# Optimization experiments

Hardware: AMD Instinct MI355X
Metric: run time of the kernel (lower is better)

The kernel has to match this reference:

```python
import jax, jax.numpy as jnp
import numpy as np
from jax import lax

KERNEL = 512

def squash(x, axis=-1):
    sn = jnp.sum(x * x, axis=axis, keepdims=True)
    scale = sn / (1.0 + sn)
    return scale * x / jnp.sqrt(sn + 1e-8)

def setup_inputs() -> dict:
    key = jax.random.key(0)
    ks = jax.random.split(key, 6)
    x = jax.random.normal(ks[0], (4096, 1, 1008), dtype=jnp.float32)
    a = jax.random.uniform(ks[1], (128, 1, 1), dtype=jnp.float32) * 5.0 + 0.1
    w = jax.random.uniform(ks[2], (128, 1, 1), dtype=jnp.float32) * 150.0 + 1.0
    conv_w = jax.random.normal(ks[3], (256, 128, 16), dtype=jnp.float32) * 0.02
    conv_b = jnp.zeros((256,), dtype=jnp.float32)
    W_caps = jax.random.normal(ks[4], (288, 4, 16, 8), dtype=jnp.float32) * 0.01
    return {"x": x, "a": a, "w": w, "conv_w": conv_w, "conv_b": conv_b, "W_caps": W_caps}

def reference(x, a, w, conv_w, conv_b, W_caps):
    # --- WavConv1d: generate wavelet weights on the fly ---
    t = jnp.linspace(-1.0, 1.0, KERNEL, dtype=jnp.float32).reshape(1, 1, KERNEL)
    a_safe = jnp.clip(a, 1e-5, None)
    t_scaled = t / a_safe
    wav_w = jnp.cos(w * t) * jnp.exp(-0.5 * t_scaled ** 2)  # [128,1,512]
    h = lax.conv_general_dilated(x, wav_w, window_strides=(16,), padding='VALID',
                                 dimension_numbers=('NCH', 'OIH', 'NCH'))  # [B,128,32]
    # --- PrimaryCaps1d ---
    p = lax.conv_general_dilated(h, conv_w, window_strides=(2,), padding='VALID',
                                 dimension_numbers=('NCH', 'OIH', 'NCH'))  # [B,256,9]
    p = p + conv_b[None, :, None]
    B = p.shape[0]
    u = squash(p.reshape(B, -1, 8))  # [B,288,8]
    # --- ClassCaps with dynamic routing ---
    # u_hat[b,c,d,o] = sum_i W_caps[c,d,o,i] * u[b,c,i]
    u_hat = jnp.einsum('cdoi,bci->bcdo', W_caps, u)  # [B,288,4,16]
    b_ij = jnp.zeros((B, u_hat.shape[1], u_hat.shape[2], 1), dtype=u_hat.dtype)
    num_routing = 3
    for i in range(num_routing):
        c_ij = jax.nn.softmax(b_ij, axis=2)                      # [B,288,4,1]
        s_j = jnp.sum(c_ij * u_hat, axis=1, keepdims=True)       # [B,1,4,16]
        v_j = squash(s_j, axis=-1)                               # [B,1,4,16]
        if i < num_routing - 1:
            agreement = jnp.sum(u_hat * v_j, axis=-1, keepdims=True)
            b_ij = b_ij + agreement
    v = jnp.squeeze(v_j, axis=1)          # [B,4,16]
    probs = jnp.linalg.norm(v, axis=-1)   # [B,4]
    return probs, jnp.squeeze(c_ij, axis=-1)  # [B,4], [B,288,4]
```

## Files before the change

### kernel.cpp

```cpp
#include <hip/hip_runtime.h>
#include <hip/hip_bf16.h>
#include <math.h>

typedef __attribute__((ext_vector_type(4))) short short4v;
typedef __attribute__((ext_vector_type(8))) short short8;
typedef __attribute__((ext_vector_type(4))) float f32x4;
typedef __attribute__((ext_vector_type(2))) float f32x2;
typedef _Float16 half8 __attribute__((ext_vector_type(8)));

#define BATCH   4096
#define XLEN    1008
#define NOC1    128
#define NPOS    32
#define NOC2    256
#define NQ      9
#define NCAPS   288
#define NDIM    8

#define BWH_OFF   0
#define BPH_OFF   131072
#define H2_OFF    1179648
#define U_OFF     34734080

static __device__ __forceinline__ short f2h(float v) {
    _Float16 h = (_Float16)v;
    return *reinterpret_cast<short*>(&h);
}

static __device__ __forceinline__ f32x2 pkfma(float a, f32x2 b, f32x2 c) {
    f32x2 av = {a, a};
    return av * b + c;
}

template <int CTRL>
static __device__ __forceinline__ float dpp_addf(float x) {
    int y = __builtin_amdgcn_update_dpp(0, __builtin_bit_cast(int, x),
                                        CTRL, 0xf, 0xf, true);
    return x + __builtin_bit_cast(float, y);
}
static __device__ __forceinline__ float rowsum16(float x) {
    x = dpp_addf<0xB1>(x);
    x = dpp_addf<0x4E>(x);
    x = dpp_addf<0x141>(x);
    x = dpp_addf<0x140>(x);
    return x;
}

__global__ __launch_bounds__(256) void k_pack(const float* __restrict__ a,
                                              const float* __restrict__ w,
                                              const float* __restrict__ cw,
                                              short* __restrict__ bwh,
                                              short* __restrict__ bph) {
    int bid = blockIdx.x;
    int tid = threadIdx.x;
    if (bid < 256) {
        int idx = bid * 256 + tid;
        int e    = idx & 7;
        int lane = (idx >> 3) & 63;
        int s    = (idx >> 9) & 15;
        int nt   = idx >> 13;
        int oc = nt * 16 + (lane & 15);
        int k  = s * 32 + (lane >> 4) * 8 + e;
        float t  = -1.0f + 2.0f * (float)k / 511.0f;
        float av = fmaxf(a[oc], 1e-5f);
        float ts = t / av;
        bwh[idx] = f2h(cosf(w[oc] * t) * expf(-0.5f * ts * ts));
    } else {
        int o = (bid - 256) * 256 + tid;
        int e    = o & 7;
        int lane = (o >> 3) & 63;
        int s    = (o >> 9) & 63;
        int nt   = o >> 15;
        int n  = nt * 16 + (lane & 15);
        int j  = lane >> 4;
        int kk = s >> 2;
        int ic = (s & 3) * 32 + j * 8 + e;
        bph[o] = f2h(cw[(n * NOC1 + ic) * 16 + kk]);
    }
}

__global__ __launch_bounds__(256, 2) void k_wavconv_mfma(
        const float* __restrict__ x,
        const short* __restrict__ bwh,
        short* __restrict__ h2) {
    __shared__ short xl[8][1512];

    int tid = threadIdx.x;
    int b0  = blockIdx.x * 8;

    for (int i4 = tid; i4 < 2016; i4 += 256) {
        int b  = i4 / 252;
        int e4 = i4 - b * 252;
        float4 v = *(const float4*)(x + (size_t)(b0 + b) * XLEN + e4 * 4);
        int i    = e4 * 4;
        int slot = i + 8 * (i >> 4);
        short4v hv;
        hv.x = f2h(v.x); hv.y = f2h(v.y); hv.z = f2h(v.z); hv.w = f2h(v.w);
        *(short4v*)&xl[b][slot] = hv;
    }
    __syncthreads();

    int lane = tid & 63;
    int w    = tid >> 6;
    int col  = lane & 15;
    int rg   = lane >> 4;

    f32x4 acc[4][8];
    f32x4 z = {0.f, 0.f, 0.f, 0.f};
#pragma unroll
    for (int tl = 0; tl < 4; ++tl)
#pragma unroll
        for (int nt = 0; nt < 8; ++nt) acc[tl][nt] = z;

    for (int s = 0; s < 16; ++s) {
        half8 Bh[8];
#pragma unroll
        for (int nt = 0; nt < 8; ++nt) {
            size_t off = ((size_t)(nt * 16 + s) * 64 + lane) * 8;
            Bh[nt] = __builtin_bit_cast(half8, *(const short8*)(bwh + off));
        }
#pragma unroll
        for (int tl = 0; tl < 4; ++tl) {
            int mt  = 4 * w + tl;
            int bl  = mt >> 1;
            int pos = (mt & 1) * 16 + col;
            int i    = (pos + 2 * s) * 16 + rg * 8;
            int slot = i + 8 * (i >> 4);
            half8 ah = __builtin_bit_cast(half8, *(const short8*)&xl[bl][slot]);
#pragma unroll
            for (int nt = 0; nt < 8; ++nt)
                acc[tl][nt] = __builtin_amdgcn_mfma_f32_16x16x32_f16(ah, Bh[nt], acc[tl][nt], 0, 0, 0);
        }
    }

#pragma unroll
    for (int tl = 0; tl < 4; ++tl) {
        int mt = 4 * w + tl;
        int b  = b0 + (mt >> 1);
        int ph = (mt & 1) * 16;
#pragma unroll
        for (int nt = 0; nt < 8; ++nt) {
            int oc = nt * 16 + col;
#pragma unroll
            for (int r = 0; r < 4; ++r) {
                int pos = ph + rg * 4 + r;
                h2[((size_t)b * NPOS + pos) * NOC1 + oc] = f2h(acc[tl][nt][r]);
            }
        }
    }
}

__global__ __launch_bounds__(512, 4) void k_conv_mfma(const short* __restrict__ h2,
                                                      const short* __restrict__ bph,
                                                      const float* __restrict__ cb,
                                                      float* __restrict__ u) {
    __shared__ char smem[66048];
    short* Ald   = (short*)smem;
    float* p_lds = (float*)smem;

    int tid  = threadIdx.x;
    int w    = tid >> 6;
    int lane = tid & 63;
    int col  = lane & 15;
    int rg   = lane >> 4;
    int b0   = blockIdx.x * 8;

    {
        const short8* src = (const short8*)(h2 + (size_t)b0 * NPOS * NOC1);
#pragma unroll
        for (int i = 0; i < 8; ++i) {
            int g    = tid + 512 * i;
            short8 v = src[g];
            int row  = g >> 4;
            int slot = (g & 15) ^ ((row >> 5) & 7);
            *(short8*)&Ald[row * 128 + slot * 8] = v;
        }
        if (tid < 32) {
            short8 zz = {0, 0, 0, 0, 0, 0, 0, 0};
            *(short8*)&Ald[4096 * 8 + tid * 8] = zz;
        }
    }
    __syncthreads();

    f32x4 acc[5][2];
    f32x4 z = {0.f, 0.f, 0.f, 0.f};
#pragma unroll
    for (int mt = 0; mt < 5; ++mt) { acc[mt][0] = z; acc[mt][1] = z; }

    int rowb[5];
#pragma unroll
    for (int mt = 0; mt < 5; ++mt) {
        int m = mt * 16 + col;
        rowb[mt] = (m & 7) * 32 + 2 * (m >> 3);
    }

    for (int s = 0; s < 64; ++s) {
        int kk    = s >> 2;
        int icb8  = (s & 3) * 4;
        short8 ar[5];
#pragma unroll
        for (int mt = 0; mt < 5; ++mt) {
            int row  = rowb[mt] + kk;
            int slot = (icb8 + rg) ^ ((row >> 5) & 7);
            ar[mt] = *(const short8*)&Ald[row * 128 + slot * 8];
        }
#pragma unroll
        for (int n = 0; n < 2; ++n) {
            size_t bo = ((size_t)((w + n * 8) * 64 + s) * 64 + lane) * 8;
            half8 Bh = __builtin_bit_cast(half8, *(const short8*)(bph + bo));
#pragma unroll
            for (int mt = 0; mt < 5; ++mt)
                acc[mt][n] = __builtin_amdgcn_mfma_f32_16x16x32_f16(
                    __builtin_bit_cast(half8, ar[mt]), Bh, acc[mt][n], 0, 0, 0);
        }
    }
    __syncthreads();

    int oc2l = w * 16 + col;
    for (int n = 0; n < 2; ++n) {
        float bias = cb[n * 128 + oc2l];
#pragma unroll
        for (int mt = 0; mt < 5; ++mt)
#pragma unroll
            for (int r = 0; r < 4; ++r) {
                int m = mt * 16 + rg * 4 + r;
                if (m < 72)
                    p_lds[(m & 7) * 1152 + oc2l * 9 + (m >> 3)] = acc[mt][n][r] + bias;
            }
        __syncthreads();
        for (int idx = tid; idx < 1152; idx += 512) {
            int lb = idx / 144;
            int cl = idx - lb * 144;
            float* ppt = &p_lds[lb * 1152 + cl * 8];
            float sn = 0.f;
#pragma unroll
            for (int i = 0; i < NDIM; ++i) sn = fmaf(ppt[i], ppt[i], sn);
            float sc = sn / (1.f + sn) / sqrtf(sn + 1e-8f);
            float* ug = u + ((size_t)(b0 + lb) * (NCAPS * NDIM) + (n * 144 + cl) * 8);
            float4 u0 = make_float4(ppt[0] * sc, ppt[1] * sc, ppt[2] * sc, ppt[3] * sc);
            float4 u1 = make_float4(ppt[4] * sc, ppt[5] * sc, ppt[6] * sc, ppt[7] * sc);
            ((float4*)ug)[0] = u0;
            ((float4*)ug)[1] = u1;
        }
        __syncthreads();
    }
}

__global__ __launch_bounds__(1024, 8) void k_routing(const float* __restrict__ u,
                                                     const float* __restrict__ Wc,
                                                     float* __restrict__ out) {
    __shared__ float b_lds[2][NCAPS * 4];
    __shared__ float c_lds[2][NCAPS * 4];
    __shared__ float s_lds[3][2][64];

    int tid = threadIdx.x;
    int b0  = blockIdx.x * 2;

    int g = tid >> 6;
    int l = tid & 63;
    int d = l >> 4;
    int o = l & 15;
    int gu = __builtin_amdgcn_readfirstlane(g);

    if (tid < 384) ((float*)s_lds)[tid] = 0.f;

    const float* ub0 = u + (size_t)(b0 + 0) * (NCAPS * NDIM) + gu * 18 * NDIM;
    const float* ub1 = u + (size_t)(b0 + 1) * (NCAPS * NDIM) + gu * 18 * NDIM;

    f32x2 uh[18];
#pragma unroll
    for (int c = 0; c < 18; ++c) {
        int cap = gu * 18 + c;
        const float4* W4 = (const float4*)(Wc + ((size_t)cap * 512) + l * 8);
        float4 A  = W4[0];
        float4 Bv = W4[1];
        f32x2 u0 = {ub0[c * 8 + 0], ub1[c * 8 + 0]};
        f32x2 u1 = {ub0[c * 8 + 1], ub1[c * 8 + 1]};
        f32x2 u2 = {ub0[c * 8 + 2], ub1[c * 8 + 2]};
        f32x2 u3 = {ub0[c * 8 + 3], ub1[c * 8 + 3]};
        f32x2 u4 = {ub0[c * 8 + 4], ub1[c * 8 + 4]};
        f32x2 u5 = {ub0[c * 8 + 5], ub1[c * 8 + 5]};
        f32x2 u6 = {ub0[c * 8 + 6], ub1[c * 8 + 6]};
        f32x2 u7 = {ub0[c * 8 + 7], ub1[c * 8 + 7]};
        f32x2 t = (f32x2){A.x, A.x} * u0;
        t = pkfma(A.y,  u1, t);
        t = pkfma(A.z,  u2, t);
        t = pkfma(A.w,  u3, t);
        t = pkfma(Bv.x, u4, t);
        t = pkfma(Bv.y, u5, t);
        t = pkfma(Bv.z, u6, t);
        t = pkfma(Bv.w, u7, t);
        uh[c] = t;
    }

    __syncthreads();

    for (int r = 0; r < 3; ++r) {
        if (r > 0) {
            __builtin_amdgcn_wave_barrier();
            for (int i = l; i < 36; i += 64) {
                int bb = (i >= 18) ? 1 : 0;
                int cl = i - bb * 18;
                int c  = gu * 18 + cl;
                float4 bv = *(const float4*)&b_lds[bb][c * 4];
                float m  = fmaxf(fmaxf(bv.x, bv.y), fmaxf(bv.z, bv.w));
                float e0 = expf(bv.x - m), e1 = expf(bv.y - m);
                float e2 = expf(bv.z - m), e3 = expf(bv.w - m);
                float inv = 1.f / (e0 + e1 + e2 + e3);
                e0 *= inv; e1 *= inv; e2 *= inv; e3 *= inv;
                *(float4*)&c_lds[bb][c * 4] = make_float4(e0, e1, e2, e3);
                if (r == 2) {
                    *(float4*)(out + 16384 + ((size_t)(b0 + bb) * NCAPS + c) * 4) =
                        make_float4(e0, e1, e2, e3);
                }
            }
            __builtin_amdgcn_wave_barrier();
        }

        f32x2 p = {0.f, 0.f};
        if (r == 0) {
#pragma unroll
            for (int c = 0; c < 18; ++c)
                p = pkfma(0.25f, uh[c], p);
        } else {
#pragma unroll
            for (int c = 0; c < 18; ++c) {
                f32x2 c2 = {c_lds[0][(g * 18 + c) * 4 + d],
                            c_lds[1][(g * 18 + c) * 4 + d]};
                p = c2 * uh[c] + p;
            }
        }
        atomicAdd(&s_lds[r][0][l], p.x);
        atomicAdd(&s_lds[r][1][l], p.y);
        __syncthreads();

        float sv0 = s_lds[r][0][l];
        float sv1 = s_lds[r][1][l];
        float sq0 = rowsum16(sv0 * sv0);
        float sq1 = rowsum16(sv1 * sv1);
        float sc0 = sq0 / (1.f + sq0) / sqrtf(sq0 + 1e-8f);
        float sc1 = sq1 / (1.f + sq1) / sqrtf(sq1 + 1e-8f);
        float v0 = sv0 * sc0;
        float v1 = sv1 * sc1;

        if (r == 2) {
            float vv0 = rowsum16(v0 * v0);
            float vv1 = rowsum16(v1 * v1);
            if (g == 0 && o == 0) {
                out[(size_t)(b0 + 0) * 4 + d] = sqrtf(vv0);
                out[(size_t)(b0 + 1) * 4 + d] = sqrtf(vv1);
            }
        } else {
            f32x2 v01 = {v0, v1};
#pragma unroll
            for (int c = 0; c < 18; ++c) {
                f32x2 t2 = uh[c] * v01;
                float t0 = rowsum16(t2.x);
                float t1 = rowsum16(t2.y);
                if (o == 0) {
                    int idx = (g * 18 + c) * 4 + d;
                    if (r == 0) {
                        b_lds[0][idx] = t0;
                        b_lds[1][idx] = t1;
                    } else {
                        b_lds[0][idx] += t0;
                        b_lds[1][idx] += t1;
                    }
                }
            }
        }
    }
}

extern "C" void kernel_launch(void* const* d_in, const int* in_sizes, int n_in,
                              void* d_out, int out_size, void* d_ws, size_t ws_size,
                              hipStream_t stream) {
    const float* x      = (const float*)d_in[0];
    const float* a      = (const float*)d_in[1];
    const float* w      = (const float*)d_in[2];
    const float* conv_w = (const float*)d_in[3];
    const float* conv_b = (const float*)d_in[4];
    const float* W_caps = (const float*)d_in[5];
    float* out = (float*)d_out;
    char* ws   = (char*)d_ws;

    short*  bwh = (short*)(ws + BWH_OFF);
    short*  bph = (short*)(ws + BPH_OFF);
    short*  h2  = (short*)(ws + H2_OFF);
    float*  u   = (float*)(ws + U_OFF);

    k_pack<<<2304, 256, 0, stream>>>(a, w, conv_w, bwh, bph);
    k_wavconv_mfma<<<BATCH / 8, 256, 0, stream>>>(x, bwh, h2);
    k_conv_mfma<<<BATCH / 8, 512, 0, stream>>>(h2, bph, conv_b, u);
    k_routing<<<BATCH / 2, 1024, 0, stream>>>(u, W_caps, out);
}
```

Baseline: 271.8 us.

## Transpose u to capsule-major layout, widen wavconv blocks, replace LDS atomics with partial sums

The wavconv kernel now uses 512 threads per block, with each wave owning one batch element instead of four tiles. That halves the accumulator registers per thread and raises occupancy, at the cost of more redundant B-fragment loads per block. The primary-caps output u is stored transposed, as [cap*8+i][batch], so the routing kernel can load adjacent batch pairs as one vector. In exchange, the conv kernel's writes become strided scatters. Routing also replaces the LDS atomicAdd reduction with per-thread partial buffers summed by each lane, removing the zero-init and the initial barrier but using more shared memory.

```diff
diff --git a/kernel.cpp b/kernel.cpp
--- a/kernel.cpp
+++ b/kernel.cpp
@@ -79,7 +79,7 @@
     }
 }
 
-__global__ __launch_bounds__(256, 2) void k_wavconv_mfma(
+__global__ __launch_bounds__(512, 4) void k_wavconv_mfma(
         const float* __restrict__ x,
         const short* __restrict__ bwh,
         short* __restrict__ h2) {
@@ -88,7 +88,7 @@
     int tid = threadIdx.x;
     int b0  = blockIdx.x * 8;
 
-    for (int i4 = tid; i4 < 2016; i4 += 256) {
+    for (int i4 = tid; i4 < 2016; i4 += 512) {
         int b  = i4 / 252;
         int e4 = i4 - b * 252;
         float4 v = *(const float4*)(x + (size_t)(b0 + b) * XLEN + e4 * 4);
@@ -105,10 +105,10 @@
     int col  = lane & 15;
     int rg   = lane >> 4;
 
-    f32x4 acc[4][8];
+    f32x4 acc[2][8];
     f32x4 z = {0.f, 0.f, 0.f, 0.f};
 #pragma unroll
-    for (int tl = 0; tl < 4; ++tl)
+    for (int tl = 0; tl < 2; ++tl)
 #pragma unroll
         for (int nt = 0; nt < 8; ++nt) acc[tl][nt] = z;
 
@@ -120,24 +120,21 @@
             Bh[nt] = __builtin_bit_cast(half8, *(const short8*)(bwh + off));
         }
 #pragma unroll
-        for (int tl = 0; tl < 4; ++tl) {
-            int mt  = 4 * w + tl;
-            int bl  = mt >> 1;
-            int pos = (mt & 1) * 16 + col;
+        for (int tl = 0; tl < 2; ++tl) {
+            int pos  = tl * 16 + col;
             int i    = (pos + 2 * s) * 16 + rg * 8;
             int slot = i + 8 * (i >> 4);
-            half8 ah = __builtin_bit_cast(half8, *(const short8*)&xl[bl][slot]);
+            half8 ah = __builtin_bit_cast(half8, *(const short8*)&xl[w][slot]);
 #pragma unroll
             for (int nt = 0; nt < 8; ++nt)
                 acc[tl][nt] = __builtin_amdgcn_mfma_f32_16x16x32_f16(ah, Bh[nt], acc[tl][nt], 0, 0, 0);
         }
     }
 
-#pragma unroll
-    for (int tl = 0; tl < 4; ++tl) {
-        int mt = 4 * w + tl;
-        int b  = b0 + (mt >> 1);
-        int ph = (mt & 1) * 16;
+    int b = b0 + w;
+#pragma unroll
+    for (int tl = 0; tl < 2; ++tl) {
+        int ph = tl * 16;
 #pragma unroll
         for (int nt = 0; nt < 8; ++nt) {
             int oc = nt * 16 + col;
@@ -153,7 +150,7 @@
 __global__ __launch_bounds__(512, 4) void k_conv_mfma(const short* __restrict__ h2,
                                                       const short* __restrict__ bph,
                                                       const float* __restrict__ cb,
-                                                      float* __restrict__ u) {
+                                                      float* __restrict__ u_tr) {
     __shared__ char smem[66048];
     short* Ald   = (short*)smem;
     float* p_lds = (float*)smem;
@@ -229,29 +226,29 @@
             }
         __syncthreads();
         for (int idx = tid; idx < 1152; idx += 512) {
-            int lb = idx / 144;
-            int cl = idx - lb * 144;
+            int cl = idx >> 3;
+            int lb = idx & 7;
             float* ppt = &p_lds[lb * 1152 + cl * 8];
             float sn = 0.f;
 #pragma unroll
             for (int i = 0; i < NDIM; ++i) sn = fmaf(ppt[i], ppt[i], sn);
             float sc = sn / (1.f + sn) / sqrtf(sn + 1e-8f);
-            float* ug = u + ((size_t)(b0 + lb) * (NCAPS * NDIM) + (n * 144 + cl) * 8);
-            float4 u0 = make_float4(ppt[0] * sc, ppt[1] * sc, ppt[2] * sc, ppt[3] * sc);
-            float4 u1 = make_float4(ppt[4] * sc, ppt[5] * sc, ppt[6] * sc, ppt[7] * sc);
-            ((float4*)ug)[0] = u0;
-            ((float4*)ug)[1] = u1;
+            int cap = n * 144 + cl;
+            float* ug = u_tr + ((size_t)cap * 8) * BATCH + b0 + lb;
+#pragma unroll
+            for (int i = 0; i < NDIM; ++i)
+                ug[(size_t)i * BATCH] = ppt[i] * sc;
         }
         __syncthreads();
     }
 }
 
-__global__ __launch_bounds__(1024, 8) void k_routing(const float* __restrict__ u,
+__global__ __launch_bounds__(1024, 8) void k_routing(const float* __restrict__ u_tr,
                                                      const float* __restrict__ Wc,
                                                      float* __restrict__ out) {
     __shared__ float b_lds[2][NCAPS * 4];
     __shared__ float c_lds[2][NCAPS * 4];
-    __shared__ float s_lds[3][2][64];
+    __shared__ f32x2 part3[3][1024];
 
     int tid = threadIdx.x;
     int b0  = blockIdx.x * 2;
@@ -262,10 +259,7 @@
     int o = l & 15;
     int gu = __builtin_amdgcn_readfirstlane(g);
 
-    if (tid < 384) ((float*)s_lds)[tid] = 0.f;
-
-    const float* ub0 = u + (size_t)(b0 + 0) * (NCAPS * NDIM) + gu * 18 * NDIM;
-    const float* ub1 = u + (size_t)(b0 + 1) * (NCAPS * NDIM) + gu * 18 * NDIM;
+    const float* ub = u_tr + (size_t)gu * 18 * 8 * BATCH + b0;
 
     f32x2 uh[18];
 #pragma unroll
@@ -274,14 +268,15 @@
         const float4* W4 = (const float4*)(Wc + ((size_t)cap * 512) + l * 8);
         float4 A  = W4[0];
         float4 Bv = W4[1];
-        f32x2 u0 = {ub0[c * 8 + 0], ub1[c * 8 + 0]};
-        f32x2 u1 = {ub0[c * 8 + 1], ub1[c * 8 + 1]};
-        f32x2 u2 = {ub0[c * 8 + 2], ub1[c * 8 + 2]};
-        f32x2 u3 = {ub0[c * 8 + 3], ub1[c * 8 + 3]};
-        f32x2 u4 = {ub0[c * 8 + 4], ub1[c * 8 + 4]};
-        f32x2 u5 = {ub0[c * 8 + 5], ub1[c * 8 + 5]};
-        f32x2 u6 = {ub0[c * 8 + 6], ub1[c * 8 + 6]};
-        f32x2 u7 = {ub0[c * 8 + 7], ub1[c * 8 + 7]};
+        const float* up = ub + (size_t)c * 8 * BATCH;
+        f32x2 u0 = *(const f32x2*)(up + 0 * BATCH);
+        f32x2 u1 = *(const f32x2*)(up + 1 * BATCH);
+        f32x2 u2 = *(const f32x2*)(up + 2 * BATCH);
+        f32x2 u3 = *(const f32x2*)(up + 3 * BATCH);
+        f32x2 u4 = *(const f32x2*)(up + 4 * BATCH);
+        f32x2 u5 = *(const f32x2*)(up + 5 * BATCH);
+        f32x2 u6 = *(const f32x2*)(up + 6 * BATCH);
+        f32x2 u7 = *(const f32x2*)(up + 7 * BATCH);
         f32x2 t = (f32x2){A.x, A.x} * u0;
         t = pkfma(A.y,  u1, t);
         t = pkfma(A.z,  u2, t);
@@ -292,8 +287,6 @@
         t = pkfma(Bv.w, u7, t);
         uh[c] = t;
     }
-
-    __syncthreads();
 
     for (int r = 0; r < 3; ++r) {
         if (r > 0) {
@@ -330,18 +323,18 @@
                 p = c2 * uh[c] + p;
             }
         }
-        atomicAdd(&s_lds[r][0][l], p.x);
-        atomicAdd(&s_lds[r][1][l], p.y);
+        part3[r][tid] = p;
         __syncthreads();
 
-        float sv0 = s_lds[r][0][l];
-        float sv1 = s_lds[r][1][l];
-        float sq0 = rowsum16(sv0 * sv0);
-        float sq1 = rowsum16(sv1 * sv1);
+        f32x2 sv = {0.f, 0.f};
+#pragma unroll
+        for (int k = 0; k < 16; ++k) sv += part3[r][l + 64 * k];
+        float sq0 = rowsum16(sv.x * sv.x);
+        float sq1 = rowsum16(sv.y * sv.y);
         float sc0 = sq0 / (1.f + sq0) / sqrtf(sq0 + 1e-8f);
         float sc1 = sq1 / (1.f + sq1) / sqrtf(sq1 + 1e-8f);
-        float v0 = sv0 * sc0;
-        float v1 = sv1 * sc1;
+        float v0 = sv.x * sc0;
+        float v1 = sv.y * sc1;
 
         if (r == 2) {
             float vv0 = rowsum16(v0 * v0);
@@ -390,7 +383,7 @@
     float*  u   = (float*)(ws + U_OFF);
 
     k_pack<<<2304, 256, 0, stream>>>(a, w, conv_w, bwh, bph);
-    k_wavconv_mfma<<<BATCH / 8, 256, 0, stream>>>(x, bwh, h2);
+    k_wavconv_mfma<<<BATCH / 8, 512, 0, stream>>>(x, bwh, h2);
     k_conv_mfma<<<BATCH / 8, 512, 0, stream>>>(h2, bph, conv_b, u);
     k_routing<<<BATCH / 2, 1024, 0, stream>>>(u, W_caps, out);
 }
```

Result: slower. 439.3 us (+61.6%).
